# Kernel optimization log

Measured on AMD Instinct MI355X. Metric: run time of the kernel, lower is better.

## Reference

```python
import jax, jax.numpy as jnp
from jax import lax
import numpy as np

KS = 15          # dark-channel window
PAD = (KS - 1) // 2
TEMP = 10000.0   # positional encoding temperature
NPF = 32         # max(num_pos_feats_x, y, z)
EPS = 1e-6


def _conv1x1(x, w, b):
    # x: [B,C,H,W], w: [O,C], b: [O]
    return jnp.einsum('bchw,oc->bohw', x, w) + b[None, :, None, None]


def _conv2s2(x, w, b):
    # kernel 2, stride 2, no padding; w: [O,I,2,2]
    y = lax.conv_general_dilated(x, w, (2, 2), 'VALID',
                                 dimension_numbers=('NCHW', 'OIHW', 'NCHW'))
    return y + b[None, :, None, None]


def _lrelu(x):
    return jnp.where(x >= 0, x, 0.1 * x)


def _resize(x, h, w):
    return jax.image.resize(x, (x.shape[0], x.shape[1], h, w), method='bilinear')


def _dark_channel(x):
    # min over channels, reflect pad, 15x15 sliding min (== unfold+min in torch)
    dm = jnp.min(x, axis=1, keepdims=True)  # [B,1,H,W]
    dm = jnp.pad(dm, ((0, 0), (0, 0), (PAD, PAD), (PAD, PAD)), mode='reflect')
    return lax.reduce_window(dm, jnp.inf, lax.min,
                             (1, 1, KS, KS), (1, 1, 1, 1), 'VALID')


def _sincos(e, d, dim_t):
    # e: [B,H,W] -> [B,H,W,d] with interleaved sin/cos (torch stack+flatten)
    p = e[..., None] / dim_t[:d]
    return jnp.stack((jnp.sin(p[..., 0::2]), jnp.cos(p[..., 1::2])),
                     axis=4).reshape(e.shape + (d,))


def _pos_encoding(x, dark):
    B, _, H, W = x.shape
    scale = 2.0 * np.pi
    yv = jnp.arange(H, dtype=jnp.float32)
    xv = jnp.arange(W, dtype=jnp.float32)
    ye = jnp.broadcast_to((yv / (yv[-1] + EPS) * scale)[None, :, None], (B, H, W))
    xe = jnp.broadcast_to((xv / (xv[-1] + EPS) * scale)[None, None, :], (B, H, W))
    z = dark[:, 0]
    ze = z / (jnp.max(z, axis=(1, 2), keepdims=True) + EPS) * scale
    dim_t = TEMP ** (2.0 * (jnp.arange(NPF, dtype=jnp.float32) // 2) / NPF)
    pos_x = _sincos(xe, 16, dim_t)
    pos_y = _sincos(ye, 16, dim_t)
    pos_z = _sincos(ze, 32, dim_t)
    return jnp.concatenate((pos_x, pos_y, pos_z), axis=3).transpose(0, 3, 1, 2)


def _forward(x, w_cf1, b_cf1, w_e1, b_e1, w_e2, b_e2, w_d1, b_d1, w_d2, b_d2,
             w_pha1, b_pha1, w_pha2, b_pha2, w_amp1, b_amp1, w_amp2, b_amp2,
             w_spat1, b_spat1, w_spat2, b_spat2, w_u1, b_u1, w_u2, b_u2,
             w_u3, b_u3, w_u4, b_u4, w_cf2, b_cf2, w_cf3, b_cf3):
    xori = x
    dark = _dark_channel(1.0 - x)            # DCP of inverted image [B,1,512,512]
    ape = _pos_encoding(x, dark) + _conv1x1(x, w_cf1, b_cf1)  # [B,64,H,W]

    x_f = _conv1x1(_conv1x1(x, w_e1, b_e1), w_e2, b_e2)       # [B,64,512,512]
    x_d1 = _conv2s2(x_f, w_d1, b_d1)                          # [B,128,256,256]
    x_d2 = _conv2s2(x_d1, w_d2, b_d2)                         # [B,256,128,128]
    Hd, Wd = x_d2.shape[2], x_d2.shape[3]

    x_freq = jnp.fft.rfft2(x_d2)             # norm='backward' (default)
    x_pha = jnp.angle(x_freq)
    x_amp = jnp.abs(x_freq)
    # phase branch is computed but unused downstream (matches original code)
    x_pha = _conv1x1(_lrelu(_conv1x1(x_pha, w_pha1, b_pha1)), w_pha2, b_pha2)
    x_amp = _conv1x1(_lrelu(_conv1x1(x_amp, w_amp1, b_amp1)), w_amp2, b_amp2)
    x_four = jnp.fft.irfft2(lax.complex(x_amp * jnp.cos(x_amp),
                                        x_amp * jnp.sin(x_amp)), s=(Hd, Wd))
    x_four = _conv1x1(_resize(x_four, x_d1.shape[2], x_d1.shape[3]), w_u1, b_u1)
    x_four = _conv1x1(_resize(x_four, x_f.shape[2], x_f.shape[3]), w_u2, b_u2)

    x_spat = _conv1x1(_lrelu(_conv1x1(x_d2, w_spat1, b_spat1)), w_spat2, b_spat2)
    x_spat = _conv1x1(_resize(x_spat, x_d1.shape[2], x_d1.shape[3]), w_u3, b_u3)
    x_spat = _conv1x1(_resize(x_spat, x_f.shape[2], x_f.shape[3]), w_u4, b_u4)
    x_spat = x_spat * ape

    four_spa = jnp.concatenate((x_four, x_spat), axis=1)      # [B,128,512,512]
    out = _conv1x1(_conv1x1(four_spa, w_cf2, b_cf2), w_cf3, b_cf3)
    return out + xori


def setup_inputs() -> dict:
    key = jax.random.key(0)
    ks = iter(jax.random.split(key, 64))
    def W(*shape):
        return 0.02 * jax.random.normal(next(ks), shape, dtype=jnp.float32)
    def Bb(n):
        return 0.01 * jax.random.normal(next(ks), (n,), dtype=jnp.float32)
    nc = 64
    inp = {'x': jax.random.uniform(next(ks), (1, 3, 512, 512), dtype=jnp.float32)}
    inp.update(w_cf1=W(nc, 3), b_cf1=Bb(nc))
    inp.update(w_e1=W(nc // 8, 3), b_e1=Bb(nc // 8))
    inp.update(w_e2=W(nc, nc // 8), b_e2=Bb(nc))
    inp.update(w_d1=W(2 * nc, nc, 2, 2), b_d1=Bb(2 * nc))
    inp.update(w_d2=W(4 * nc, 2 * nc, 2, 2), b_d2=Bb(4 * nc))
    for nm in ('pha', 'amp', 'spat'):
        inp['w_%s1' % nm] = W(4 * nc, 4 * nc); inp['b_%s1' % nm] = Bb(4 * nc)
        inp['w_%s2' % nm] = W(4 * nc, 4 * nc); inp['b_%s2' % nm] = Bb(4 * nc)
    inp.update(w_u1=W(2 * nc, 4 * nc), b_u1=Bb(2 * nc))
    inp.update(w_u2=W(nc, 2 * nc), b_u2=Bb(nc))
    inp.update(w_u3=W(2 * nc, 4 * nc), b_u3=Bb(2 * nc))
    inp.update(w_u4=W(nc, 2 * nc), b_u4=Bb(nc))
    inp.update(w_cf2=W(nc, 2 * nc), b_cf2=Bb(nc))
    inp.update(w_cf3=W(3, nc), b_cf3=Bb(3))
    return inp


def reference(x, w_cf1, b_cf1, w_e1, b_e1, w_e2, b_e2, w_d1, b_d1, w_d2, b_d2,
              w_pha1, b_pha1, w_pha2, b_pha2, w_amp1, b_amp1, w_amp2, b_amp2,
              w_spat1, b_spat1, w_spat2, b_spat2, w_u1, b_u1, w_u2, b_u2,
              w_u3, b_u3, w_u4, b_u4, w_cf2, b_cf2, w_cf3, b_cf3):
    return _forward(x, w_cf1, b_cf1, w_e1, b_e1, w_e2, b_e2, w_d1, b_d1,
                    w_d2, b_d2, w_pha1, b_pha1, w_pha2, b_pha2, w_amp1, b_amp1,
                    w_amp2, b_amp2, w_spat1, b_spat1, w_spat2, b_spat2,
                    w_u1, b_u1, w_u2, b_u2, w_u3, b_u3, w_u4, b_u4,
                    w_cf2, b_cf2, w_cf3, b_cf3)
```

## Files before the change

### kernel.cpp

```cpp
#include <hip/hip_runtime.h>
#include <math.h>

#define PI_F 3.14159265358979323846f
#define NPIX 262144

typedef __attribute__((ext_vector_type(8))) short sh8;
typedef __attribute__((ext_vector_type(4))) float fx4;
typedef __attribute__((ext_vector_type(4))) unsigned short ush4;

__device__ __forceinline__ unsigned short f2bf(float v) {
    unsigned u = __float_as_uint(v);
    return (unsigned short)((u + 0x7FFFu + ((u >> 16) & 1)) >> 16);
}
__device__ __forceinline__ float bf2f(unsigned short h) {
    return __uint_as_float((unsigned)h << 16);
}

__device__ __forceinline__ int refl512(int t) {
    if (t < 0) t = -t;
    if (t > 511) t = 1022 - t;
    return t;
}

__global__ __launch_bounds__(256) void k_dark(const float* __restrict__ x, float* __restrict__ dark,
                                              int* __restrict__ gmax) {
    __shared__ float rm[15][512];
    __shared__ float hm[15][512];
    __shared__ float red[256];
    int i = blockIdx.x, tid = threadIdx.x;
    for (int idx = tid; idx < 15 * 512; idx += 256) {
        int rr = idx >> 9, j = idx & 511;
        int row = refl512(i - 7 + rr);
        int p = (row << 9) + j;
        rm[rr][j] = 1.0f - fmaxf(x[p], fmaxf(x[p + NPIX], x[p + 2 * NPIX]));
    }
    __syncthreads();
    for (int idx = tid; idx < 15 * 512; idx += 256) {
        int rr = idx >> 9, j = idx & 511;
        float m = 1e30f;
        #pragma unroll
        for (int d = -7; d <= 7; d++) m = fminf(m, rm[rr][refl512(j + d)]);
        hm[rr][j] = m;
    }
    __syncthreads();
    float best = -1e30f;
    #pragma unroll
    for (int h = 0; h < 2; h++) {
        int j = tid + h * 256;
        float m = 1e30f;
        #pragma unroll
        for (int rr = 0; rr < 15; rr++) m = fminf(m, hm[rr][j]);
        dark[(i << 9) + j] = m;
        best = fmaxf(best, m);
    }
    red[tid] = best;
    __syncthreads();
    for (int s = 128; s > 0; s >>= 1) {
        if (tid < s) red[tid] = fmaxf(red[tid], red[tid + s]);
        __syncthreads();
    }
    if (tid == 0) atomicMax(gmax, __float_as_int(red[0]));
}

__device__ __forceinline__ void prep_one(const float* __restrict__ w, unsigned short* __restrict__ h,
                                         unsigned short* __restrict__ l, int N, int K, int cshift, int idx) {
    if (idx >= N * K) return;
    int n = idx / K, kord = idx - n * K;
    int ksrc = kord;
    if (cshift) {
        int dydx = kord >> cshift, c = kord & ((1 << cshift) - 1);
        ksrc = c * 4 + dydx;
    }
    float v = w[n * K + ksrc];
    unsigned short hb = f2bf(v);
    h[idx] = hb;
    if (l) l[idx] = f2bf(v - bf2f(hb));
}

__global__ __launch_bounds__(256) void k_prepA(
    const float* __restrict__ w_d2, unsigned short* __restrict__ d2h, unsigned short* __restrict__ d2l,
    const float* __restrict__ w_a1, unsigned short* __restrict__ a1h, unsigned short* __restrict__ a1l,
    const float* __restrict__ w_a2, unsigned short* __restrict__ a2h, unsigned short* __restrict__ a2l,
    const float* __restrict__ w_s1, unsigned short* __restrict__ s1h,
    const float* __restrict__ w_u3, const float* __restrict__ w_u4, float* __restrict__ Uf,
    unsigned short* __restrict__ BfH, unsigned short* __restrict__ BfL,
    unsigned short* __restrict__ BfcH, unsigned short* __restrict__ BfcL,
    unsigned short* __restrict__ BicH, unsigned short* __restrict__ BicL,
    float* __restrict__ Birf,
    float* __restrict__ zbias, int* __restrict__ gmax) {
    int b = blockIdx.x, tid = threadIdx.x;
    if (b == 0 && tid == 0) gmax[0] = 0;
    if (b < 512)       { prep_one(w_d2, d2h, d2l, 256, 512, 7, b * 256 + tid); return; }
    else if (b < 768)  { prep_one(w_a1, a1h, a1l, 256, 256, 0, (b - 512) * 256 + tid); return; }
    else if (b < 1024) { prep_one(w_a2, a2h, a2l, 256, 256, 0, (b - 768) * 256 + tid); return; }
    else if (b < 1280) { prep_one(w_s1, s1h, nullptr, 256, 256, 0, (b - 1024) * 256 + tid); return; }
    else if (b >= 2000) {
        int idx = (b - 2000) * 256 + tid;
        int n = idx >> 8, j = idx & 255;
        float s = 0.f;
        #pragma unroll 16
        for (int o = 0; o < 128; o++) s += w_u4[n * 128 + o] * w_u3[o * 256 + j];
        Uf[idx] = s;
        return;
    }
    int idx = (b - 1280) * 256 + tid;
    if (idx < 256) zbias[idx] = 0.f;
    const float w0 = 2.f * PI_F / 128.f;
    float v;
    unsigned short *H, *L;
    int off;
    if (idx < 32768) {
        int n = idx >> 7, k = idx & 127;
        int t = n & 127, r = (t * k) & 127;
        float s_, c_; sincosf(w0 * r, &s_, &c_);
        v = (n < 128) ? c_ : -s_;
        H = BfH; L = BfL; off = idx;
    } else if (idx < 98304) {
        int i = idx - 32768;
        int n = i >> 8, j = i & 255;
        int t = n & 127, r = (t * (j & 127)) & 127;
        float s_, c_; sincosf(w0 * r, &s_, &c_);
        v = (n < 128) ? ((j < 128) ? c_ : s_) : ((j < 128) ? -s_ : c_);
        H = BfcH; L = BfcL; off = i;
    } else if (idx < 163840) {
        int i = idx - 98304;
        int n = i >> 8, j = i & 255;
        int t = n & 127, r = (t * (j & 127)) & 127;
        float s_, c_; sincosf(w0 * r, &s_, &c_);
        v = ((n < 128) ? ((j < 128) ? c_ : -s_) : ((j < 128) ? s_ : c_)) * (1.f / 128.f);
        H = BicH; L = BicL; off = i;
    } else if (idx < 184320) {
        int i2 = idx - 163840;
        int col = i2 / 160, j = i2 - col * 160;
        if (j == 0) v = 1.f / 128.f;
        else if (j < 64)  { int r = (j * col) & 127; float s_, c_; sincosf(w0 * r, &s_, &c_); v = 2.f * c_ / 128.f; }
        else if (j == 64) v = (col & 1) ? -1.f / 128.f : 1.f / 128.f;
        else if (j >= 66 && j <= 128) { int k = j - 65; int r = (k * col) & 127; float s_, c_; sincosf(w0 * r, &s_, &c_); v = -2.f * s_ / 128.f; }
        else v = 0.f;
        Birf[j * 128 + col] = v;
        return;
    } else return;
    unsigned short hb = f2bf(v);
    H[off] = hb;
    L[off] = f2bf(v - bf2f(hb));
}

__global__ __launch_bounds__(256) void k_prepB(
    const float* __restrict__ Uf,
    const float* __restrict__ w_e1, const float* __restrict__ b_e1,
    const float* __restrict__ w_e2, const float* __restrict__ b_e2,
    const float* __restrict__ w_d1, const float* __restrict__ b_d1,
    unsigned short* __restrict__ d1ch, float* __restrict__ b1c,
    const float* __restrict__ w_u4, const float* __restrict__ b_u3, const float* __restrict__ b_u4,
    const float* __restrict__ wsp2, const float* __restrict__ bsp2,
    unsigned short* __restrict__ Wg, float* __restrict__ bgc,
    const float* __restrict__ w2, const float* __restrict__ b2,
    const float* __restrict__ w3, const float* __restrict__ b3,
    const float* __restrict__ wu2, const float* __restrict__ bu2,
    const float* __restrict__ wu1, const float* __restrict__ bu1,
    float* __restrict__ Wc, float* __restrict__ bc,
    float* __restrict__ W21c, float* __restrict__ b21c) {
    int b = blockIdx.x, tid = threadIdx.x;
    if (b < 16) {
        __shared__ float E[192];
        if (tid < 192) {
            int o = tid / 3, ci = tid - o * 3;
            float s = 0.f;
            #pragma unroll
            for (int r = 0; r < 8; r++) s += w_e2[o * 8 + r] * w_e1[r * 3 + ci];
            E[tid] = s;
        }
        __syncthreads();
        int idx = b * 256 + tid;
        int n = idx >> 5, k = idx & 31;
        float s = 0.f;
        if (k < 12) {
            int dydx = k / 3, ci = k - dydx * 3;
            #pragma unroll 16
            for (int o = 0; o < 64; o++) s += w_d1[n * 256 + o * 4 + dydx] * E[o * 3 + ci];
        }
        d1ch[idx] = f2bf(s);
    } else if (b == 16) {
        __shared__ float f[64];
        if (tid < 64) {
            int o = tid;
            float s = b_e2[o];
            #pragma unroll
            for (int r = 0; r < 8; r++) s += w_e2[o * 8 + r] * b_e1[r];
            f[o] = s;
        }
        __syncthreads();
        if (tid < 128) {
            float s = b_d1[tid];
            #pragma unroll 8
            for (int o = 0; o < 64; o++) {
                float fo = f[o];
                #pragma unroll
                for (int dydx = 0; dydx < 4; dydx++) s += w_d1[tid * 256 + o * 4 + dydx] * fo;
            }
            b1c[tid] = s;
        }
    } else if (b == 17) {
        __shared__ float sWc[384], sW2c[384];
        if (tid < 128) {
            int j = tid;
            for (int r = 0; r < 3; r++) {
                float s = 0.f;
                #pragma unroll 16
                for (int o = 0; o < 64; o++) s += w3[r * 64 + o] * w2[o * 128 + j];
                sWc[r * 128 + j] = s;
                Wc[r * 128 + j] = s;
            }
            if (j < 3) {
                float s = b3[j];
                #pragma unroll 16
                for (int o = 0; o < 64; o++) s += w3[j * 64 + o] * b2[o];
                bc[j] = s;
            }
        }
        __syncthreads();
        if (tid < 128) {
            int j = tid;
            for (int r = 0; r < 3; r++) {
                float s = 0.f;
                #pragma unroll 16
                for (int o = 0; o < 64; o++) s += sWc[r * 128 + o] * wu2[o * 128 + j];
                sW2c[r * 128 + j] = s;
            }
        }
        __syncthreads();
        if (tid < 256) {
            int j = tid;
            for (int r = 0; r < 3; r++) {
                float s = 0.f;
                #pragma unroll 16
                for (int o = 0; o < 128; o++) s += sW2c[r * 128 + o] * wu1[o * 256 + j];
                W21c[r * 256 + j] = s;
            }
        }
        if (tid < 3) {
            float s = 0.f;
            #pragma unroll 16
            for (int o = 0; o < 128; o++) s += sW2c[tid * 128 + o] * bu1[o];
            #pragma unroll 16
            for (int o = 0; o < 64; o++)  s += sWc[tid * 128 + o] * bu2[o];
            b21c[tid] = s;
        }
    } else {
        int n = b - 18;
        __shared__ float u[256], red[256];
        u[tid] = Uf[n * 256 + tid];
        __syncthreads();
        float s = 0.f;
        #pragma unroll 16
        for (int o = 0; o < 256; o++) s += u[o] * wsp2[o * 256 + tid];
        Wg[n * 256 + tid] = f2bf(s);
        float rv = u[tid] * bsp2[tid];
        if (tid < 128) rv += w_u4[n * 128 + tid] * b_u3[tid];
        red[tid] = rv;
        __syncthreads();
        for (int st = 128; st > 0; st >>= 1) {
            if (tid < st) red[tid] += red[tid + st];
            __syncthreads();
        }
        if (tid == 0) bgc[n] = b_u4[n] + red[0];
    }
}

template<int AMODE, int SPLIT, int LRELU, int TSTORE, int ABF16, int CBF16>
__global__ __launch_bounds__(256) void k_mmcf(const void* __restrict__ Asrc_,
                                              const unsigned short* __restrict__ Bh,
                                              const unsigned short* __restrict__ Bl,
                                              const float* __restrict__ bias, void* __restrict__ C_,
                                              int M, int N, int K, int cshift, int wshift, int srcW,
                                              int gy) {
    const float* Af = (const float*)Asrc_;
    const unsigned short* A16 = (const unsigned short*)Asrc_;
    float* Cf = (float*)C_;
    unsigned short* C16 = (unsigned short*)C_;
    __shared__ unsigned short AhS[128 * 40];
    __shared__ unsigned short BhS[64 * 40];
    __shared__ unsigned short AlS[SPLIT ? 128 * 40 : 8];
    __shared__ unsigned short BlS[SPLIT ? 64 * 40 : 8];
    int tid = threadIdx.x;
    int nwg = (int)gridDim.x;
    int bid = blockIdx.x;
    int qq = nwg >> 3, rr = nwg & 7;
    int xcd = bid & 7, ixw = bid >> 3;
    int work = (xcd < rr) ? (xcd * (qq + 1) + ixw) : (rr * (qq + 1) + (xcd - rr) * qq + ixw);
    int bx = work / gy;
    int by = work - bx * gy;
    int m0 = bx * 128;
    int n0 = by * 64;
    int wave = tid >> 6, lane = tid & 63;
    int wm = (wave >> 1) * 64, wn = (wave & 1) * 32;
    int l15 = lane & 15, quad = lane >> 4;
    int lk = quad * 8, lk4 = quad * 4;
    fx4 acc[4][2];
    #pragma unroll
    for (int a = 0; a < 4; a++)
        #pragma unroll
        for (int b = 0; b < 2; b++)
            acc[a][b] = (fx4){0.f, 0.f, 0.f, 0.f};

    int mm = tid & 127;
    int kpb = tid >> 7;
    int gm = m0 + mm;
    int oj = 0, oi = 0, cA = 0, kfA = 0, tauA = 0;
    size_t abase = 0;
    if (AMODE == 1) { oj = gm & ((1 << wshift) - 1); oi = gm >> wshift; }
    if (AMODE == 2) { oj = gm & 255; oi = gm >> 8; }
    if (AMODE == 3) abase = (size_t)gm * K;
    if (AMODE == 7) { cA = gm / 65; kfA = gm - cA * 65; }
    if (AMODE == 9) { cA = gm / 65; kfA = gm - cA * 65; }

    for (int kb = 0; kb < K; kb += 32) {
        if (AMODE == 3 && ABF16 && !SPLIT) {
            #pragma unroll
            for (int half = 0; half < 2; half++) {
                sh8 hv = *(const sh8*)(const void*)&A16[abase + kb + kpb * 16 + half * 8];
                *(sh8*)(void*)&AhS[mm * 40 + (kpb * 2 + half) * 8] = hv;
            }
        } else {
            #pragma unroll
            for (int half = 0; half < 2; half++) {
                sh8 hv, lv;
                #pragma unroll
                for (int tt = 0; tt < 4; tt++) {
                    int kp = kpb * 8 + half * 4 + tt;
                    int k0 = kb + kp * 2;
                    unsigned short h0, h1;
                    if (ABF16) {
                        size_t ad0, ad1;
                        if (AMODE == 0) {
                            ad0 = (size_t)k0 * M + gm;
                            ad1 = ad0 + M;
                        } else if (AMODE == 1) {
                            int c = k0 & ((1 << cshift) - 1);
                            int dydx = k0 >> cshift;
                            int dy = dydx >> 1, dx = dydx & 1;
                            size_t pix = (size_t)(2 * oi + dy) * srcW + (2 * oj + dx);
                            size_t plane = (size_t)srcW * srcW;
                            ad0 = (size_t)c * plane + pix;
                            ad1 = ad0 + plane;
                        } else if (AMODE == 3) {
                            ad0 = abase + k0;
                            ad1 = ad0 + 1;
                        } else {
                            int t0 = k0 & 127, hf = k0 >> 7;
                            ad0 = (size_t)(cA * 128 + t0) * 256 + hf * 128 + kfA;
                            ad1 = ad0 + 256;
                        }
                        h0 = A16[ad0];
                        h1 = A16[ad1];
                    } else {
                        float a0, a1;
                        if (AMODE == 2) {
                            if (k0 < 12) {
                                int d0 = k0 / 3, c0 = k0 - d0 * 3;
                                int k1 = k0 + 1;
                                int d1x = k1 / 3, c1 = k1 - d1x * 3;
                                a0 = Af[(size_t)c0 * NPIX + (size_t)(2 * oi + (d0 >> 1)) * 512 + 2 * oj + (d0 & 1)];
                                a1 = Af[(size_t)c1 * NPIX + (size_t)(2 * oi + (d1x >> 1)) * 512 + 2 * oj + (d1x & 1)];
                            } else { a0 = 0.f; a1 = 0.f; }
                        } else if (AMODE == 9) {
                            size_t ad = (size_t)cA * 16640 + (size_t)k0 * 65 + kfA;
                            float re0 = Af[ad], im0 = Af[ad + 2129920];
                            float re1 = Af[ad + 65], im1 = Af[ad + 65 + 2129920];
                            a0 = sqrtf(re0 * re0 + im0 * im0);
                            a1 = sqrtf(re1 * re1 + im1 * im1);
                        } else {
                            size_t ad0 = (size_t)k0 * M + gm;
                            a0 = Af[ad0];
                            a1 = Af[ad0 + M];
                        }
                        h0 = f2bf(a0);
                        h1 = f2bf(a1);
                        if (SPLIT) {
                            lv[tt * 2] = (short)f2bf(a0 - bf2f(h0));
                            lv[tt * 2 + 1] = (short)f2bf(a1 - bf2f(h1));
                        }
                    }
                    hv[tt * 2] = (short)h0;
                    hv[tt * 2 + 1] = (short)h1;
                }
                int coff = (kpb * 2 + half) * 8;
                *(sh8*)(void*)&AhS[mm * 40 + coff] = hv;
                if (SPLIT) *(sh8*)(void*)&AlS[mm * 40 + coff] = lv;
            }
        }
        {
            int n = tid >> 2, seg = tid & 3;
            size_t gb = (size_t)(n0 + n) * K + kb + seg * 8;
            *(sh8*)(void*)&BhS[n * 40 + seg * 8] = *(const sh8*)(const void*)&Bh[gb];
            if (SPLIT) *(sh8*)(void*)&BlS[n * 40 + seg * 8] = *(const sh8*)(const void*)&Bl[gb];
        }
        __syncthreads();
        sh8 af[4], bf[2], afl[4], bfl[2];
        #pragma unroll
        for (int mt = 0; mt < 4; mt++) {
            af[mt] = *(const sh8*)(const void*)&AhS[(wm + mt * 16 + l15) * 40 + lk];
            if (SPLIT) afl[mt] = *(const sh8*)(const void*)&AlS[(wm + mt * 16 + l15) * 40 + lk];
        }
        #pragma unroll
        for (int nt = 0; nt < 2; nt++) {
            bf[nt] = *(const sh8*)(const void*)&BhS[(wn + nt * 16 + l15) * 40 + lk];
            if (SPLIT) bfl[nt] = *(const sh8*)(const void*)&BlS[(wn + nt * 16 + l15) * 40 + lk];
        }
        #pragma unroll
        for (int mt = 0; mt < 4; mt++)
            #pragma unroll
            for (int nt = 0; nt < 2; nt++) {
                acc[mt][nt] = __builtin_amdgcn_mfma_f32_16x16x32_bf16(af[mt], bf[nt], acc[mt][nt], 0, 0, 0);
                if (SPLIT) {
                    acc[mt][nt] = __builtin_amdgcn_mfma_f32_16x16x32_bf16(af[mt], bfl[nt], acc[mt][nt], 0, 0, 0);
                    acc[mt][nt] = __builtin_amdgcn_mfma_f32_16x16x32_bf16(afl[mt], bf[nt], acc[mt][nt], 0, 0, 0);
                }
            }
        __syncthreads();
    }
    #pragma unroll
    for (int nt = 0; nt < 2; nt++) {
        int n = n0 + wn + nt * 16 + l15;
        float bs = bias[n];
        #pragma unroll
        for (int mt = 0; mt < 4; mt++) {
            int mbase = m0 + wm + mt * 16 + lk4;
            if (TSTORE) {
                #pragma unroll
                for (int r = 0; r < 4; r++) {
                    float q = acc[mt][nt][r] + bs;
                    if (LRELU) q = (q < 0.f) ? 0.1f * q : q;
                    if (CBF16) C16[(size_t)(mbase + r) * N + n] = f2bf(q);
                    else       Cf[(size_t)(mbase + r) * N + n] = q;
                }
            } else if (CBF16) {
                ush4 v;
                #pragma unroll
                for (int r = 0; r < 4; r++) {
                    float q = acc[mt][nt][r] + bs;
                    if (LRELU) q = (q < 0.f) ? 0.1f * q : q;
                    v[r] = f2bf(q);
                }
                *(ush4*)(void*)&C16[(size_t)n * M + mbase] = v;
            } else {
                float4 v;
                float* vp = (float*)&v;
                #pragma unroll
                for (int r = 0; r < 4; r++) {
                    float q = acc[mt][nt][r] + bs;
                    if (LRELU) q = (q < 0.f) ? 0.1f * q : q;
                    vp[r] = q;
                }
                *(float4*)&Cf[(size_t)n * M + mbase] = v;
            }
        }
    }
}

__global__ __launch_bounds__(256) void k_zbuild(const float* __restrict__ A2, unsigned short* __restrict__ Z) {
    int idx = blockIdx.x * 256 + threadIdx.x;
    int ct = idx / 65, kf = idx - ct * 65;
    int c = ct >> 7, t = ct & 127;
    float a = A2[idx];
    float s_, c_;
    sincosf(a, &s_, &c_);
    size_t m = (size_t)c * 65 + kf;
    Z[(size_t)t * 16640 + m] = f2bf(a * c_);
    Z[2129920 + (size_t)t * 16640 + m] = f2bf(a * s_);
}

__global__ __launch_bounds__(256) void k_pfold(const unsigned short* __restrict__ I1T,
                                               const float* __restrict__ W21c, float* __restrict__ P) {
    __shared__ float wa[768];
    int kf = blockIdx.x, tid = threadIdx.x;
    for (int t = tid; t < 768; t += 256) wa[t] = W21c[t];
    __syncthreads();
    float a0 = 0.f, a1 = 0.f, a2 = 0.f;
    #pragma unroll 4
    for (int c = 0; c < 256; c++) {
        float v = bf2f(I1T[(size_t)(c * 65 + kf) * 256 + tid]);
        a0 += wa[c] * v;
        a1 += wa[256 + c] * v;
        a2 += wa[512 + c] * v;
    }
    P[(size_t)(0 * 65 + kf) * 256 + tid] = a0;
    P[(size_t)(1 * 65 + kf) * 256 + tid] = a1;
    P[(size_t)(2 * 65 + kf) * 256 + tid] = a2;
}

__global__ __launch_bounds__(128) void k_h3f(const float* __restrict__ P, const float* __restrict__ Birf,
                                             const float* __restrict__ b21c, float* __restrict__ h3s) {
    __shared__ float sp[390];
    __shared__ float bs[3];
    int tau = blockIdx.x, col = threadIdx.x;
    for (int t = col; t < 390; t += 128) {
        int r = t / 130, rem = t - r * 130;
        int hf = rem / 65, kf = rem - hf * 65;
        sp[t] = P[(size_t)(r * 65 + kf) * 256 + hf * 128 + tau];
    }
    if (col < 3) bs[col] = b21c[col];
    __syncthreads();
    float f0 = 0.f, f1 = 0.f, f2 = 0.f;
    for (int k0 = 0; k0 < 130; k0++) {
        float w = Birf[k0 * 128 + col];
        int hf = (k0 >= 65) ? 1 : 0;
        int base = hf ? (65 + k0 - 65) : k0;
        f0 += w * sp[base];
        f1 += w * sp[130 + base];
        f2 += w * sp[260 + base];
    }
    size_t q = (size_t)tau * 128 + col;
    h3s[q]         = f0 + bs[0];
    h3s[16384 + q] = f1 + bs[1];
    h3s[32768 + q] = f2 + bs[2];
}

__global__ __launch_bounds__(256) void k_final(const float* __restrict__ x,
                                               const float* __restrict__ dark, const int* __restrict__ gmax,
                                               const float* __restrict__ wcf1, const float* __restrict__ bcf1,
                                               const float* __restrict__ Wc, const float* __restrict__ bc,
                                               const float* __restrict__ g4s, const float* __restrict__ h3s,
                                               float* __restrict__ out) {
    __shared__ float idimt[32], w1[192], b1[64], wb[192], bcs[3], posy[16];
    __shared__ float gyr[64][68];
    __shared__ float hyr[3][68];
    int tid = threadIdx.x;
    int bid = blockIdx.x;
    int i = bid >> 1;
    int j0 = (bid & 1) << 8;
    int j = j0 + tid;
    int p = (i << 9) + j;

    const float scale = 2.f * PI_F;
    float inv511 = scale / (511.f + 1e-6f);
    float ye = (float)i * inv511;

    if (tid < 32) idimt[tid] = 1.f / powf(10000.f, (float)(2 * (tid >> 1)) / 32.f);
    if (tid < 192) w1[tid] = wcf1[tid];
    if (tid < 64) b1[tid] = bcf1[tid];
    if (tid < 192) { int r = tid / 64, c = tid - (tid / 64) * 64; wb[tid] = Wc[r * 128 + 64 + c]; }
    if (tid < 3) bcs[tid] = bc[tid];
    __syncthreads();
    if (tid >= 32 && tid < 48) {
        int c = tid - 32;
        float e = ye * idimt[c];
        posy[c] = ((c & 1) == 0) ? __sinf(e) : __cosf(e);
    }

    int ky = i >> 2, ry = i & 3;
    int ym = (ky > 0) ? ky - 1 : 0, yp = (ky < 127) ? ky + 1 : 127;
    float wy0 = (ry == 0) ? .375f : (ry == 1) ? .1875f : (ry == 2) ? .0625f : 0.f;
    float wy1 = (ry == 0 || ry == 3) ? .625f : .75f;
    float wy2 = (ry == 0) ? 0.f : (ry == 1) ? .0625f : (ry == 2) ? .1875f : .375f;
    int base = j0 >> 2;
    int r0 = ym * 128, r1 = ky * 128, r2 = yp * 128;
    for (int idx = tid; idx < 64 * 66; idx += 256) {
        int c = idx / 66, t = idx - c * 66;
        int col = base - 1 + t;
        col = (col < 0) ? 0 : (col > 127) ? 127 : col;
        const float* gp = g4s + (size_t)c * 16384;
        gyr[c][t] = wy0 * gp[r0 + col] + wy1 * gp[r1 + col] + wy2 * gp[r2 + col];
    }
    for (int idx = tid; idx < 3 * 66; idx += 256) {
        int c = idx / 66, t = idx - c * 66;
        int col = base - 1 + t;
        col = (col < 0) ? 0 : (col > 127) ? 127 : col;
        const float* hp = h3s + (size_t)c * 16384;
        hyr[c][t] = wy0 * hp[r0 + col] + wy1 * hp[r1 + col] + wy2 * hp[r2 + col];
    }
    __syncthreads();

    float xe = (float)j * inv511;
    float gm = __int_as_float(gmax[0]);
    float ze = dark[p] / (gm + 1e-6f) * scale;
    float x0 = x[p], x1 = x[p + NPIX], x2 = x[p + 2 * NPIX];

    int rx = j & 3;
    int tx = tid >> 2;
    float wx0 = (rx == 0) ? .375f : (rx == 1) ? .1875f : (rx == 2) ? .0625f : 0.f;
    float wx1 = (rx == 0 || rx == 3) ? .625f : .75f;
    float wx2 = (rx == 0) ? 0.f : (rx == 1) ? .0625f : (rx == 2) ? .1875f : .375f;

    float a0 = 0.f, a1 = 0.f, a2 = 0.f;
    #pragma unroll 1
    for (int c = 0; c < 64; c++) {
        float pos;
        if (c < 16)      { float e = xe * idimt[c];      pos = ((c & 1) == 0) ? __sinf(e) : __cosf(e); }
        else if (c < 32) { pos = posy[c - 16]; }
        else             { float e = ze * idimt[c - 32]; pos = ((c & 1) == 0) ? __sinf(e) : __cosf(e); }
        float ape = pos + w1[c * 3] * x0 + w1[c * 3 + 1] * x1 + w1[c * 3 + 2] * x2 + b1[c];
        float gv = wx0 * gyr[c][tx] + wx1 * gyr[c][tx + 1] + wx2 * gyr[c][tx + 2];
        float s = gv * ape;
        a0 += wb[c] * s; a1 += wb[64 + c] * s; a2 += wb[128 + c] * s;
    }
    float f0 = wx0 * hyr[0][tx] + wx1 * hyr[0][tx + 1] + wx2 * hyr[0][tx + 2];
    float f1 = wx0 * hyr[1][tx] + wx1 * hyr[1][tx + 1] + wx2 * hyr[1][tx + 2];
    float f2 = wx0 * hyr[2][tx] + wx1 * hyr[2][tx + 1] + wx2 * hyr[2][tx + 2];
    out[p]            = a0 + f0 + bcs[0] + x0;
    out[NPIX + p]     = a1 + f1 + bcs[1] + x1;
    out[2 * NPIX + p] = a2 + f2 + bcs[2] + x2;
}

extern "C" void kernel_launch(void* const* d_in, const int* in_sizes, int n_in,
                              void* d_out, int out_size, void* d_ws, size_t ws_size,
                              hipStream_t stream) {
    const float* x      = (const float*)d_in[0];
    const float* w_cf1  = (const float*)d_in[1];  const float* b_cf1 = (const float*)d_in[2];
    const float* w_e1   = (const float*)d_in[3];  const float* b_e1  = (const float*)d_in[4];
    const float* w_e2   = (const float*)d_in[5];  const float* b_e2  = (const float*)d_in[6];
    const float* w_d1   = (const float*)d_in[7];  const float* b_d1  = (const float*)d_in[8];
    const float* w_d2   = (const float*)d_in[9];  const float* b_d2  = (const float*)d_in[10];
    const float* w_amp1 = (const float*)d_in[15]; const float* b_amp1 = (const float*)d_in[16];
    const float* w_amp2 = (const float*)d_in[17]; const float* b_amp2 = (const float*)d_in[18];
    const float* w_sp1  = (const float*)d_in[19]; const float* b_sp1  = (const float*)d_in[20];
    const float* w_sp2  = (const float*)d_in[21]; const float* b_sp2  = (const float*)d_in[22];
    const float* w_u1   = (const float*)d_in[23]; const float* b_u1   = (const float*)d_in[24];
    const float* w_u2   = (const float*)d_in[25]; const float* b_u2   = (const float*)d_in[26];
    const float* w_u3   = (const float*)d_in[27]; const float* b_u3   = (const float*)d_in[28];
    const float* w_u4   = (const float*)d_in[29]; const float* b_u4   = (const float*)d_in[30];
    const float* w_cf2  = (const float*)d_in[31]; const float* b_cf2  = (const float*)d_in[32];
    const float* w_cf3  = (const float*)d_in[33]; const float* b_cf3  = (const float*)d_in[34];
    float* out = (float*)d_out;

    char* ws = (char*)d_ws;
    constexpr size_t MiB = 1ull << 20;
    float*  dark   = (float*)(ws + 0 * MiB);
    int*    gmax   = (int*)  (ws + 2 * MiB);
    float*  Wc     = (float*)(ws + 2 * MiB + 1024);
    float*  bc     = (float*)(ws + 2 * MiB + 2560);
    float*  W21c   = (float*)(ws + 2 * MiB + 4096);
    float*  b21c   = (float*)(ws + 2 * MiB + 7168);
    unsigned short* d1ch = (unsigned short*)(ws + 3 * MiB);
    float*  b1c    = (float*)(ws + 3 * MiB + 16384);
    float*  Uf     = (float*)(ws + 3 * MiB + 32768);
    unsigned short* Wg = (unsigned short*)(ws + 3 * MiB + 131072);
    float*  bgc    = (float*)(ws + 3 * MiB + 196608);
    unsigned short* xd1 = (unsigned short*)(ws + 67 * MiB);
    unsigned short* xd2 = (unsigned short*)(ws + 99 * MiB);
    unsigned short* F1T = (unsigned short*)(ws + 115 * MiB);
    float*  F2C    = (float*)(ws + 147 * MiB);
    float*  A1     = (float*)(ws + 173 * MiB);
    float*  A2     = (float*)(ws + 182 * MiB);
    unsigned short* Zbuf = (unsigned short*)(ws + 115 * MiB);
    unsigned short* I1T  = (unsigned short*)(ws + 132 * MiB);
    float*  P      = (float*)(ws + 149 * MiB);
    float*  h3s    = (float*)(ws + 11 * MiB);
    unsigned short* s1 = (unsigned short*)(ws + 31 * MiB);
    float*  g4s    = (float*)(ws + 87 * MiB);
    unsigned short* wb16 = (unsigned short*)(ws + 192 * MiB);
    unsigned short* d2h = wb16 + 65536,   * d2l = wb16 + 196608;
    unsigned short* a1h = wb16 + 327680,  * a1l = wb16 + 393216;
    unsigned short* a2h = wb16 + 458752,  * a2l = wb16 + 524288;
    unsigned short* s1h = wb16 + 589824;
    unsigned short* BfH = wb16 + 786432,  * BfL = wb16 + 819200;
    unsigned short* BfcH = wb16 + 851968, * BfcL = wb16 + 917504;
    unsigned short* BicH = wb16 + 983040, * BicL = wb16 + 1048576;
    float* zbias = (float*)(ws + 195 * MiB + 512 * 1024);
    float* Birf  = (float*)(ws + 196 * MiB);

    k_prepA<<<2064, 256, 0, stream>>>(w_d2, d2h, d2l, w_amp1, a1h, a1l, w_amp2, a2h, a2l, w_sp1, s1h,
                                      w_u3, w_u4, Uf,
                                      BfH, BfL, BfcH, BfcL, BicH, BicL, Birf, zbias, gmax);
    k_dark<<<512, 256, 0, stream>>>(x, dark, gmax);
    k_prepB<<<82, 256, 0, stream>>>(Uf,
                                    w_e1, b_e1, w_e2, b_e2, w_d1, b_d1, d1ch, b1c,
                                    w_u4, b_u3, b_u4, w_sp2, b_sp2, Wg, bgc,
                                    w_cf2, b_cf2, w_cf3, b_cf3, w_u2, b_u2, w_u1, b_u1,
                                    Wc, bc, W21c, b21c);

    k_mmcf<2, 0, 0, 0, 0, 1><<<1024, 256, 0, stream>>>(x, d1ch, nullptr, b1c, xd1, 65536, 128, 32, 0, 0, 0, 2);
    k_mmcf<1, 0, 0, 0, 1, 1><<<512, 256, 0, stream>>>(xd1, d2h, nullptr, b_d2, xd2, 16384, 256, 512, 7, 7, 256, 4);

    k_mmcf<3, 0, 0, 1, 1, 1><<<1024, 256, 0, stream>>>(xd2, BfH, nullptr, zbias, F1T, 32768, 256, 128, 0, 0, 0, 4);
    k_mmcf<7, 0, 0, 0, 1, 0><<<520, 256, 0, stream>>>(F1T, BfcH, nullptr, zbias, F2C, 16640, 256, 256, 0, 0, 0, 4);
    k_mmcf<9, 1, 1, 0, 0, 0><<<260, 256, 0, stream>>>(F2C, a1h, a1l, b_amp1, A1, 8320, 256, 256, 0, 0, 0, 4);
    k_mmcf<0, 1, 0, 0, 0, 0><<<260, 256, 0, stream>>>(A1, a2h, a2l, b_amp2, A2, 8320, 256, 256, 0, 0, 0, 4);
    k_zbuild<<<8320, 256, 0, stream>>>(A2, Zbuf);
    k_mmcf<0, 0, 0, 1, 1, 1><<<520, 256, 0, stream>>>(Zbuf, BicH, nullptr, zbias, I1T, 16640, 256, 256, 0, 0, 0, 4);

    k_pfold<<<65, 256, 0, stream>>>(I1T, W21c, P);
    k_h3f<<<128, 128, 0, stream>>>(P, Birf, b21c, h3s);

    k_mmcf<0, 0, 1, 0, 1, 1><<<512, 256, 0, stream>>>(xd2, s1h, nullptr, b_sp1, s1, 16384, 256, 256, 0, 0, 0, 4);
    k_mmcf<0, 0, 0, 0, 1, 0><<<128, 256, 0, stream>>>(s1, Wg, nullptr, bgc, g4s, 16384, 64, 256, 0, 0, 0, 1);

    k_final<<<1024, 256, 0, stream>>>(x, dark, gmax, w_cf1, b_cf1, Wc, bc, g4s, h3s, out);
}
```

Before: 345.0 us.

## Merge prep and dark-channel kernels, pair independent GEMMs into combined launches

Merges the two weight-prep kernels and the dark-channel kernel into one launch, inlining the Uf product into the bgc blocks. The dark channel now takes the column min first, then a 1-D horizontal min, and writes per-block maxima instead of using a global atomic. The max reduction moves into an extra block of the d1 GEMM kernel. Independent GEMMs (F1T with the spatial s1, F2C with g4s) are paired into shared launches to cut launch count and fill idle CUs, at the cost of uneven block mixes and a single shared-memory size per kernel.

```diff
diff --git a/kernel.cpp b/kernel.cpp
--- a/kernel.cpp
+++ b/kernel.cpp
@@ -20,46 +20,6 @@
     if (t < 0) t = -t;
     if (t > 511) t = 1022 - t;
     return t;
-}
-
-__global__ __launch_bounds__(256) void k_dark(const float* __restrict__ x, float* __restrict__ dark,
-                                              int* __restrict__ gmax) {
-    __shared__ float rm[15][512];
-    __shared__ float hm[15][512];
-    __shared__ float red[256];
-    int i = blockIdx.x, tid = threadIdx.x;
-    for (int idx = tid; idx < 15 * 512; idx += 256) {
-        int rr = idx >> 9, j = idx & 511;
-        int row = refl512(i - 7 + rr);
-        int p = (row << 9) + j;
-        rm[rr][j] = 1.0f - fmaxf(x[p], fmaxf(x[p + NPIX], x[p + 2 * NPIX]));
-    }
-    __syncthreads();
-    for (int idx = tid; idx < 15 * 512; idx += 256) {
-        int rr = idx >> 9, j = idx & 511;
-        float m = 1e30f;
-        #pragma unroll
-        for (int d = -7; d <= 7; d++) m = fminf(m, rm[rr][refl512(j + d)]);
-        hm[rr][j] = m;
-    }
-    __syncthreads();
-    float best = -1e30f;
-    #pragma unroll
-    for (int h = 0; h < 2; h++) {
-        int j = tid + h * 256;
-        float m = 1e30f;
-        #pragma unroll
-        for (int rr = 0; rr < 15; rr++) m = fminf(m, hm[rr][j]);
-        dark[(i << 9) + j] = m;
-        best = fmaxf(best, m);
-    }
-    red[tid] = best;
-    __syncthreads();
-    for (int s = 128; s > 0; s >>= 1) {
-        if (tid < s) red[tid] = fmaxf(red[tid], red[tid + s]);
-        __syncthreads();
-    }
-    if (tid == 0) atomicMax(gmax, __float_as_int(red[0]));
 }
 
 __device__ __forceinline__ void prep_one(const float* __restrict__ w, unsigned short* __restrict__ h,
@@ -77,81 +37,22 @@
     if (l) l[idx] = f2bf(v - bf2f(hb));
 }
 
-__global__ __launch_bounds__(256) void k_prepA(
+__global__ __launch_bounds__(256) void k_prep(
+    const float* __restrict__ x, float* __restrict__ dark, float* __restrict__ blockmax,
     const float* __restrict__ w_d2, unsigned short* __restrict__ d2h, unsigned short* __restrict__ d2l,
     const float* __restrict__ w_a1, unsigned short* __restrict__ a1h, unsigned short* __restrict__ a1l,
     const float* __restrict__ w_a2, unsigned short* __restrict__ a2h, unsigned short* __restrict__ a2l,
     const float* __restrict__ w_s1, unsigned short* __restrict__ s1h,
-    const float* __restrict__ w_u3, const float* __restrict__ w_u4, float* __restrict__ Uf,
     unsigned short* __restrict__ BfH, unsigned short* __restrict__ BfL,
     unsigned short* __restrict__ BfcH, unsigned short* __restrict__ BfcL,
     unsigned short* __restrict__ BicH, unsigned short* __restrict__ BicL,
-    float* __restrict__ Birf,
-    float* __restrict__ zbias, int* __restrict__ gmax) {
-    int b = blockIdx.x, tid = threadIdx.x;
-    if (b == 0 && tid == 0) gmax[0] = 0;
-    if (b < 512)       { prep_one(w_d2, d2h, d2l, 256, 512, 7, b * 256 + tid); return; }
-    else if (b < 768)  { prep_one(w_a1, a1h, a1l, 256, 256, 0, (b - 512) * 256 + tid); return; }
-    else if (b < 1024) { prep_one(w_a2, a2h, a2l, 256, 256, 0, (b - 768) * 256 + tid); return; }
-    else if (b < 1280) { prep_one(w_s1, s1h, nullptr, 256, 256, 0, (b - 1024) * 256 + tid); return; }
-    else if (b >= 2000) {
-        int idx = (b - 2000) * 256 + tid;
-        int n = idx >> 8, j = idx & 255;
-        float s = 0.f;
-        #pragma unroll 16
-        for (int o = 0; o < 128; o++) s += w_u4[n * 128 + o] * w_u3[o * 256 + j];
-        Uf[idx] = s;
-        return;
-    }
-    int idx = (b - 1280) * 256 + tid;
-    if (idx < 256) zbias[idx] = 0.f;
-    const float w0 = 2.f * PI_F / 128.f;
-    float v;
-    unsigned short *H, *L;
-    int off;
-    if (idx < 32768) {
-        int n = idx >> 7, k = idx & 127;
-        int t = n & 127, r = (t * k) & 127;
-        float s_, c_; sincosf(w0 * r, &s_, &c_);
-        v = (n < 128) ? c_ : -s_;
-        H = BfH; L = BfL; off = idx;
-    } else if (idx < 98304) {
-        int i = idx - 32768;
-        int n = i >> 8, j = i & 255;
-        int t = n & 127, r = (t * (j & 127)) & 127;
-        float s_, c_; sincosf(w0 * r, &s_, &c_);
-        v = (n < 128) ? ((j < 128) ? c_ : s_) : ((j < 128) ? -s_ : c_);
-        H = BfcH; L = BfcL; off = i;
-    } else if (idx < 163840) {
-        int i = idx - 98304;
-        int n = i >> 8, j = i & 255;
-        int t = n & 127, r = (t * (j & 127)) & 127;
-        float s_, c_; sincosf(w0 * r, &s_, &c_);
-        v = ((n < 128) ? ((j < 128) ? c_ : -s_) : ((j < 128) ? s_ : c_)) * (1.f / 128.f);
-        H = BicH; L = BicL; off = i;
-    } else if (idx < 184320) {
-        int i2 = idx - 163840;
-        int col = i2 / 160, j = i2 - col * 160;
-        if (j == 0) v = 1.f / 128.f;
-        else if (j < 64)  { int r = (j * col) & 127; float s_, c_; sincosf(w0 * r, &s_, &c_); v = 2.f * c_ / 128.f; }
-        else if (j == 64) v = (col & 1) ? -1.f / 128.f : 1.f / 128.f;
-        else if (j >= 66 && j <= 128) { int k = j - 65; int r = (k * col) & 127; float s_, c_; sincosf(w0 * r, &s_, &c_); v = -2.f * s_ / 128.f; }
-        else v = 0.f;
-        Birf[j * 128 + col] = v;
-        return;
-    } else return;
-    unsigned short hb = f2bf(v);
-    H[off] = hb;
-    L[off] = f2bf(v - bf2f(hb));
-}
-
-__global__ __launch_bounds__(256) void k_prepB(
-    const float* __restrict__ Uf,
+    float* __restrict__ Birf, float* __restrict__ zbias,
     const float* __restrict__ w_e1, const float* __restrict__ b_e1,
     const float* __restrict__ w_e2, const float* __restrict__ b_e2,
     const float* __restrict__ w_d1, const float* __restrict__ b_d1,
     unsigned short* __restrict__ d1ch, float* __restrict__ b1c,
-    const float* __restrict__ w_u4, const float* __restrict__ b_u3, const float* __restrict__ b_u4,
+    const float* __restrict__ w_u3, const float* __restrict__ w_u4,
+    const float* __restrict__ b_u3, const float* __restrict__ b_u4,
     const float* __restrict__ wsp2, const float* __restrict__ bsp2,
     unsigned short* __restrict__ Wg, float* __restrict__ bgc,
     const float* __restrict__ w2, const float* __restrict__ b2,
@@ -160,9 +61,56 @@
     const float* __restrict__ wu1, const float* __restrict__ bu1,
     float* __restrict__ Wc, float* __restrict__ bc,
     float* __restrict__ W21c, float* __restrict__ b21c) {
+    __shared__ float smem[8448];
     int b = blockIdx.x, tid = threadIdx.x;
-    if (b < 16) {
-        __shared__ float E[192];
+    if (b < 512)       { prep_one(w_d2, d2h, d2l, 256, 512, 7, b * 256 + tid); return; }
+    else if (b < 768)  { prep_one(w_a1, a1h, a1l, 256, 256, 0, (b - 512) * 256 + tid); return; }
+    else if (b < 1024) { prep_one(w_a2, a2h, a2l, 256, 256, 0, (b - 768) * 256 + tid); return; }
+    else if (b < 1280) { prep_one(w_s1, s1h, nullptr, 256, 256, 0, (b - 1024) * 256 + tid); return; }
+    else if (b < 2000) {
+        int idx = (b - 1280) * 256 + tid;
+        if (idx < 256) zbias[idx] = 0.f;
+        const float w0 = 2.f * PI_F / 128.f;
+        float v;
+        unsigned short *H, *L;
+        int off;
+        if (idx < 32768) {
+            int n = idx >> 7, k = idx & 127;
+            int t = n & 127, r = (t * k) & 127;
+            float s_, c_; sincosf(w0 * r, &s_, &c_);
+            v = (n < 128) ? c_ : -s_;
+            H = BfH; L = BfL; off = idx;
+        } else if (idx < 98304) {
+            int i = idx - 32768;
+            int n = i >> 8, j = i & 255;
+            int t = n & 127, r = (t * (j & 127)) & 127;
+            float s_, c_; sincosf(w0 * r, &s_, &c_);
+            v = (n < 128) ? ((j < 128) ? c_ : s_) : ((j < 128) ? -s_ : c_);
+            H = BfcH; L = BfcL; off = i;
+        } else if (idx < 163840) {
+            int i = idx - 98304;
+            int n = i >> 8, j = i & 255;
+            int t = n & 127, r = (t * (j & 127)) & 127;
+            float s_, c_; sincosf(w0 * r, &s_, &c_);
+            v = ((n < 128) ? ((j < 128) ? c_ : -s_) : ((j < 128) ? s_ : c_)) * (1.f / 128.f);
+            H = BicH; L = BicL; off = i;
+        } else if (idx < 184320) {
+            int i2 = idx - 163840;
+            int col = i2 / 160, j = i2 - col * 160;
+            if (j == 0) v = 1.f / 128.f;
+            else if (j < 64)  { int r = (j * col) & 127; float s_, c_; sincosf(w0 * r, &s_, &c_); v = 2.f * c_ / 128.f; }
+            else if (j == 64) v = (col & 1) ? -1.f / 128.f : 1.f / 128.f;
+            else if (j >= 66 && j <= 128) { int k = j - 65; int r = (k * col) & 127; float s_, c_; sincosf(w0 * r, &s_, &c_); v = -2.f * s_ / 128.f; }
+            else v = 0.f;
+            Birf[j * 128 + col] = v;
+            return;
+        } else return;
+        unsigned short hb = f2bf(v);
+        H[off] = hb;
+        L[off] = f2bf(v - bf2f(hb));
+    }
+    else if (b < 2016) {
+        float* E = smem;
         if (tid < 192) {
             int o = tid / 3, ci = tid - o * 3;
             float s = 0.f;
@@ -171,7 +119,7 @@
             E[tid] = s;
         }
         __syncthreads();
-        int idx = b * 256 + tid;
+        int idx = (b - 2000) * 256 + tid;
         int n = idx >> 5, k = idx & 31;
         float s = 0.f;
         if (k < 12) {
@@ -180,8 +128,8 @@
             for (int o = 0; o < 64; o++) s += w_d1[n * 256 + o * 4 + dydx] * E[o * 3 + ci];
         }
         d1ch[idx] = f2bf(s);
-    } else if (b == 16) {
-        __shared__ float f[64];
+    } else if (b == 2016) {
+        float* f = smem;
         if (tid < 64) {
             int o = tid;
             float s = b_e2[o];
@@ -200,8 +148,9 @@
             }
             b1c[tid] = s;
         }
-    } else if (b == 17) {
-        __shared__ float sWc[384], sW2c[384];
+    } else if (b == 2017) {
+        float* sWc = smem;
+        float* sW2c = smem + 384;
         if (tid < 128) {
             int j = tid;
             for (int r = 0; r < 3; r++) {
@@ -246,10 +195,16 @@
             for (int o = 0; o < 64; o++)  s += sWc[tid * 128 + o] * bu2[o];
             b21c[tid] = s;
         }
-    } else {
-        int n = b - 18;
-        __shared__ float u[256], red[256];
-        u[tid] = Uf[n * 256 + tid];
+    } else if (b < 2082) {
+        int n = b - 2018;
+        float* u = smem;
+        float* red = smem + 256;
+        {
+            float s = 0.f;
+            #pragma unroll 16
+            for (int o = 0; o < 128; o++) s += w_u4[n * 128 + o] * w_u3[o * 256 + tid];
+            u[tid] = s;
+        }
         __syncthreads();
         float s = 0.f;
         #pragma unroll 16
@@ -264,27 +219,64 @@
             __syncthreads();
         }
         if (tid == 0) bgc[n] = b_u4[n] + red[0];
+    } else {
+        int i = b - 2082;
+        float* rm = smem;
+        float* cm = smem + 7680;
+        float* red = smem + 8192;
+        for (int idx = tid; idx < 15 * 512; idx += 256) {
+            int rr = idx >> 9, j = idx & 511;
+            int row = refl512(i - 7 + rr);
+            int p = (row << 9) + j;
+            rm[rr * 512 + j] = 1.0f - fmaxf(x[p], fmaxf(x[p + NPIX], x[p + 2 * NPIX]));
+        }
+        __syncthreads();
+        #pragma unroll
+        for (int h = 0; h < 2; h++) {
+            int j = tid + h * 256;
+            float m = 1e30f;
+            #pragma unroll
+            for (int rr = 0; rr < 15; rr++) m = fminf(m, rm[rr * 512 + j]);
+            cm[j] = m;
+        }
+        __syncthreads();
+        float best = -1e30f;
+        #pragma unroll
+        for (int h = 0; h < 2; h++) {
+            int j = tid + h * 256;
+            float m = 1e30f;
+            #pragma unroll
+            for (int d = -7; d <= 7; d++) m = fminf(m, cm[refl512(j + d)]);
+            dark[(i << 9) + j] = m;
+            best = fmaxf(best, m);
+        }
+        red[tid] = best;
+        __syncthreads();
+        for (int s = 128; s > 0; s >>= 1) {
+            if (tid < s) red[tid] = fmaxf(red[tid], red[tid + s]);
+            __syncthreads();
+        }
+        if (tid == 0) blockmax[i] = red[0];
     }
 }
 
 template<int AMODE, int SPLIT, int LRELU, int TSTORE, int ABF16, int CBF16>
-__global__ __launch_bounds__(256) void k_mmcf(const void* __restrict__ Asrc_,
-                                              const unsigned short* __restrict__ Bh,
-                                              const unsigned short* __restrict__ Bl,
-                                              const float* __restrict__ bias, void* __restrict__ C_,
-                                              int M, int N, int K, int cshift, int wshift, int srcW,
-                                              int gy) {
+__device__ __forceinline__ void mm_body(unsigned short* __restrict__ SH,
+                                        const void* __restrict__ Asrc_,
+                                        const unsigned short* __restrict__ Bh,
+                                        const unsigned short* __restrict__ Bl,
+                                        const float* __restrict__ bias, void* __restrict__ C_,
+                                        int M, int N, int K, int cshift, int wshift, int srcW,
+                                        int gy, int bid, int nwg) {
     const float* Af = (const float*)Asrc_;
     const unsigned short* A16 = (const unsigned short*)Asrc_;
     float* Cf = (float*)C_;
     unsigned short* C16 = (unsigned short*)C_;
-    __shared__ unsigned short AhS[128 * 40];
-    __shared__ unsigned short BhS[64 * 40];
-    __shared__ unsigned short AlS[SPLIT ? 128 * 40 : 8];
-    __shared__ unsigned short BlS[SPLIT ? 64 * 40 : 8];
+    unsigned short* AhS = SH;
+    unsigned short* BhS = SH + 5120;
+    unsigned short* AlS = SPLIT ? SH + 7680 : SH;
+    unsigned short* BlS = SPLIT ? SH + 12800 : SH;
     int tid = threadIdx.x;
-    int nwg = (int)gridDim.x;
-    int bid = blockIdx.x;
     int qq = nwg >> 3, rr = nwg & 7;
     int xcd = bid & 7, ixw = bid >> 3;
     int work = (xcd < rr) ? (xcd * (qq + 1) + ixw) : (rr * (qq + 1) + (xcd - rr) * qq + ixw);
@@ -306,7 +298,7 @@
     int mm = tid & 127;
     int kpb = tid >> 7;
     int gm = m0 + mm;
-    int oj = 0, oi = 0, cA = 0, kfA = 0, tauA = 0;
+    int oj = 0, oi = 0, cA = 0, kfA = 0;
     size_t abase = 0;
     if (AMODE == 1) { oj = gm & ((1 << wshift) - 1); oi = gm >> wshift; }
     if (AMODE == 2) { oj = gm & 255; oi = gm >> 8; }
@@ -458,6 +450,69 @@
     }
 }
 
+template<int AMODE, int SPLIT, int LRELU, int TSTORE, int ABF16, int CBF16>
+__global__ __launch_bounds__(256) void k_mmcf(const void* __restrict__ Asrc_,
+                                              const unsigned short* __restrict__ Bh,
+                                              const unsigned short* __restrict__ Bl,
+                                              const float* __restrict__ bias, void* __restrict__ C_,
+                                              int M, int N, int K, int cshift, int wshift, int srcW,
+                                              int gy) {
+    __shared__ unsigned short SH[SPLIT ? 15360 : 7680];
+    mm_body<AMODE, SPLIT, LRELU, TSTORE, ABF16, CBF16>(SH, Asrc_, Bh, Bl, bias, C_,
+                                                       M, N, K, cshift, wshift, srcW, gy,
+                                                       (int)blockIdx.x, (int)gridDim.x);
+}
+
+__global__ __launch_bounds__(256) void k_d1(const float* __restrict__ x,
+                                            const unsigned short* __restrict__ d1ch,
+                                            const float* __restrict__ b1c, unsigned short* __restrict__ xd1,
+                                            const float* __restrict__ blockmax, int* __restrict__ gmax) {
+    if (blockIdx.x == 1024) {
+        __shared__ float red[256];
+        int tid = threadIdx.x;
+        red[tid] = fmaxf(blockmax[tid], blockmax[tid + 256]);
+        __syncthreads();
+        for (int s = 128; s > 0; s >>= 1) {
+            if (tid < s) red[tid] = fmaxf(red[tid], red[tid + s]);
+            __syncthreads();
+        }
+        if (tid == 0) gmax[0] = __float_as_int(red[0]);
+        return;
+    }
+    __shared__ unsigned short SH[7680];
+    mm_body<2, 0, 0, 0, 0, 1>(SH, x, d1ch, nullptr, b1c, xd1, 65536, 128, 32, 0, 0, 0, 2,
+                              (int)blockIdx.x, 1024);
+}
+
+__global__ __launch_bounds__(256) void k_dualA(const unsigned short* __restrict__ xd2,
+                                               const unsigned short* __restrict__ BfH,
+                                               const float* __restrict__ zbias, unsigned short* __restrict__ F1T,
+                                               const unsigned short* __restrict__ s1h,
+                                               const float* __restrict__ b_sp1, unsigned short* __restrict__ s1) {
+    __shared__ unsigned short SH[7680];
+    if (blockIdx.x < 1024)
+        mm_body<3, 0, 0, 1, 1, 1>(SH, xd2, BfH, nullptr, zbias, F1T, 32768, 256, 128, 0, 0, 0, 4,
+                                  (int)blockIdx.x, 1024);
+    else
+        mm_body<0, 0, 1, 0, 1, 1>(SH, xd2, s1h, nullptr, b_sp1, s1, 16384, 256, 256, 0, 0, 0, 4,
+                                  (int)blockIdx.x - 1024, 512);
+}
+
+__global__ __launch_bounds__(256) void k_dualB(const unsigned short* __restrict__ F1T,
+                                               const unsigned short* __restrict__ BfcH,
+                                               const float* __restrict__ zbias, float* __restrict__ F2C,
+                                               const unsigned short* __restrict__ s1,
+                                               const unsigned short* __restrict__ Wg,
+                                               const float* __restrict__ bgc, float* __restrict__ g4s) {
+    __shared__ unsigned short SH[7680];
+    if (blockIdx.x < 520)
+        mm_body<7, 0, 0, 0, 1, 0>(SH, F1T, BfcH, nullptr, zbias, F2C, 16640, 256, 256, 0, 0, 0, 4,
+                                  (int)blockIdx.x, 520);
+    else
+        mm_body<0, 0, 0, 0, 1, 0>(SH, s1, Wg, nullptr, bgc, g4s, 16384, 64, 256, 0, 0, 0, 1,
+                                  (int)blockIdx.x - 520, 128);
+}
+
 __global__ __launch_bounds__(256) void k_zbuild(const float* __restrict__ A2, unsigned short* __restrict__ Z) {
     int idx = blockIdx.x * 256 + threadIdx.x;
     int ct = idx / 65, kf = idx - ct * 65;
@@ -631,9 +686,9 @@
     float*  bc     = (float*)(ws + 2 * MiB + 2560);
     float*  W21c   = (float*)(ws + 2 * MiB + 4096);
     float*  b21c   = (float*)(ws + 2 * MiB + 7168);
+    float*  blockmax = (float*)(ws + 2 * MiB + 8192);
     unsigned short* d1ch = (unsigned short*)(ws + 3 * MiB);
     float*  b1c    = (float*)(ws + 3 * MiB + 16384);
-    float*  Uf     = (float*)(ws + 3 * MiB + 32768);
     unsigned short* Wg = (unsigned short*)(ws + 3 * MiB + 131072);
     float*  bgc    = (float*)(ws + 3 * MiB + 196608);
     unsigned short* xd1 = (unsigned short*)(ws + 67 * MiB);
@@ -659,21 +714,21 @@
     float* zbias = (float*)(ws + 195 * MiB + 512 * 1024);
     float* Birf  = (float*)(ws + 196 * MiB);
 
-    k_prepA<<<2064, 256, 0, stream>>>(w_d2, d2h, d2l, w_amp1, a1h, a1l, w_amp2, a2h, a2l, w_sp1, s1h,
-                                      w_u3, w_u4, Uf,
-                                      BfH, BfL, BfcH, BfcL, BicH, BicL, Birf, zbias, gmax);
-    k_dark<<<512, 256, 0, stream>>>(x, dark, gmax);
-    k_prepB<<<82, 256, 0, stream>>>(Uf,
-                                    w_e1, b_e1, w_e2, b_e2, w_d1, b_d1, d1ch, b1c,
-                                    w_u4, b_u3, b_u4, w_sp2, b_sp2, Wg, bgc,
-                                    w_cf2, b_cf2, w_cf3, b_cf3, w_u2, b_u2, w_u1, b_u1,
-                                    Wc, bc, W21c, b21c);
-
-    k_mmcf<2, 0, 0, 0, 0, 1><<<1024, 256, 0, stream>>>(x, d1ch, nullptr, b1c, xd1, 65536, 128, 32, 0, 0, 0, 2);
+    k_prep<<<2594, 256, 0, stream>>>(
+        x, dark, blockmax,
+        w_d2, d2h, d2l, w_amp1, a1h, a1l, w_amp2, a2h, a2l, w_sp1, s1h,
+        BfH, BfL, BfcH, BfcL, BicH, BicL, Birf, zbias,
+        w_e1, b_e1, w_e2, b_e2, w_d1, b_d1, d1ch, b1c,
+        w_u3, w_u4, b_u3, b_u4, w_sp2, b_sp2, Wg, bgc,
+        w_cf2, b_cf2, w_cf3, b_cf3, w_u2, b_u2, w_u1, b_u1,
+        Wc, bc, W21c, b21c);
+
+    k_d1<<<1025, 256, 0, stream>>>(x, d1ch, b1c, xd1, blockmax, gmax);
     k_mmcf<1, 0, 0, 0, 1, 1><<<512, 256, 0, stream>>>(xd1, d2h, nullptr, b_d2, xd2, 16384, 256, 512, 7, 7, 256, 4);
 
-    k_mmcf<3, 0, 0, 1, 1, 1><<<1024, 256, 0, stream>>>(xd2, BfH, nullptr, zbias, F1T, 32768, 256, 128, 0, 0, 0, 4);
-    k_mmcf<7, 0, 0, 0, 1, 0><<<520, 256, 0, stream>>>(F1T, BfcH, nullptr, zbias, F2C, 16640, 256, 256, 0, 0, 0, 4);
+    k_dualA<<<1536, 256, 0, stream>>>(xd2, BfH, zbias, F1T, s1h, b_sp1, s1);
+    k_dualB<<<648, 256, 0, stream>>>(F1T, BfcH, zbias, F2C, s1, Wg, bgc, g4s);
+
     k_mmcf<9, 1, 1, 0, 0, 0><<<260, 256, 0, stream>>>(F2C, a1h, a1l, b_amp1, A1, 8320, 256, 256, 0, 0, 0, 4);
     k_mmcf<0, 1, 0, 0, 0, 0><<<260, 256, 0, stream>>>(A1, a2h, a2l, b_amp2, A2, 8320, 256, 256, 0, 0, 0, 4);
     k_zbuild<<<8320, 256, 0, stream>>>(A2, Zbuf);
@@ -682,8 +737,5 @@
     k_pfold<<<65, 256, 0, stream>>>(I1T, W21c, P);
     k_h3f<<<128, 128, 0, stream>>>(P, Birf, b21c, h3s);
 
-    k_mmcf<0, 0, 1, 0, 1, 1><<<512, 256, 0, stream>>>(xd2, s1h, nullptr, b_sp1, s1, 16384, 256, 256, 0, 0, 0, 4);
-    k_mmcf<0, 0, 0, 0, 1, 0><<<128, 256, 0, stream>>>(s1, Wg, nullptr, bgc, g4s, 16384, 64, 256, 0, 0, 0, 1);
-
     k_final<<<1024, 256, 0, stream>>>(x, dark, gmax, w_cf1, b_cf1, Wc, bc, g4s, h3s, out);
 }
```

Measured after the change: 314.4 us. 8.9% less time.
